# Optimization experiments

Measured on AMD Instinct MI355X. Metric: run time of the kernel, lower is better.

Reference implementation:

```python
import jax, jax.numpy as jnp
import numpy as np

N_NODES = 50000
N_EDGES = 600000
DIM = 128
VOCAB = 512
PAD_ID = 0
LN_EPS = 1e-5


def setup_inputs() -> dict:
    key = jax.random.key(0)
    ks = jax.random.split(key, 8)
    node_ids = jax.random.randint(ks[0], (N_NODES,), 0, VOCAB, dtype=jnp.int32)
    edge_index = jax.random.randint(ks[1], (2, N_EDGES), 0, N_NODES, dtype=jnp.int32)
    edge_weight = jax.random.uniform(ks[2], (N_EDGES,), dtype=jnp.float32)
    # embedding with padding row zeroed (padding_idx semantics)
    emb = jax.random.normal(ks[3], (VOCAB, DIM), dtype=jnp.float32) * 0.05
    emb = emb.at[PAD_ID].set(0.0)
    s = 1.0 / np.sqrt(DIM)
    W1 = jax.random.normal(ks[4], (DIM, DIM), dtype=jnp.float32) * s
    b1 = jnp.zeros((DIM,), jnp.float32)
    W2 = jax.random.normal(ks[5], (DIM, DIM), dtype=jnp.float32) * s
    b2 = jnp.zeros((DIM,), jnp.float32)
    return {
        "node_ids": node_ids, "edge_index": edge_index, "edge_weight": edge_weight,
        "emb": emb, "W1": W1, "b1": b1, "W2": W2, "b2": b2,
        "gamma1": jnp.ones((DIM,), jnp.float32), "beta1": jnp.zeros((DIM,), jnp.float32),
        "gamma2": jnp.ones((DIM,), jnp.float32), "beta2": jnp.zeros((DIM,), jnp.float32),
    }


def _gcn_conv(x, row, col, ew, W, b, n_nodes):
    """PyG GCNConv: normalize=True, add_self_loops=True, improved=False.
    Aggregation j->i: edge (row=src j, col=dst i)."""
    h = x @ W  # [N, out]
    # add self loops with weight 1
    loop = jnp.arange(n_nodes, dtype=row.dtype)
    row_f = jnp.concatenate([row, loop])
    col_f = jnp.concatenate([col, loop])
    ew_f = jnp.concatenate([ew, jnp.ones((n_nodes,), ew.dtype)])
    # symmetric degree normalization (deg over destination index)
    deg = jax.ops.segment_sum(ew_f, col_f, num_segments=n_nodes)
    dis = jnp.where(deg > 0, jax.lax.rsqrt(jnp.maximum(deg, 1e-12)), 0.0)
    norm = dis[row_f] * ew_f * dis[col_f]  # [E+N]
    msg = norm[:, None] * h[row_f]  # gather + scale  [E+N, out]
    out = jax.ops.segment_sum(msg, col_f, num_segments=n_nodes)  # scatter-add
    return out + b


def _layer_norm(x, gamma, beta):
    mu = jnp.mean(x, axis=-1, keepdims=True)
    var = jnp.mean(jnp.square(x - mu), axis=-1, keepdims=True)
    return (x - mu) * jax.lax.rsqrt(var + LN_EPS) * gamma + beta


def reference(node_ids, edge_index, edge_weight, emb, W1, b1, W2, b2,
              gamma1, beta1, gamma2, beta2):
    row, col = edge_index[0], edge_index[1]
    x = emb[node_ids]  # [N, D]
    x1 = _gcn_conv(x, row, col, edge_weight, W1, b1, N_NODES)
    x = _layer_norm(x + x1, gamma1, beta1)  # dropout is identity in eval
    x2 = _gcn_conv(x, row, col, edge_weight, W2, b2, N_NODES)
    x = _layer_norm(x + x2, gamma2, beta2)
    return x
```

## Files before the change

kernel.cpp:

```cpp
#include <hip/hip_runtime.h>

#define N_NODES 50000
#define N_EDGES 600000
#define DIM     128
#define VOCAB   512
#define LN_EPS  1e-5f
#define FIXS    16777216.0f

typedef unsigned int uint;
typedef unsigned long long ull;
typedef unsigned short ushort;
typedef __attribute__((ext_vector_type(8))) short s8v;
typedef __attribute__((ext_vector_type(4))) float f4v;

__device__ __forceinline__ uint f2bf(float f) {
    uint u = __float_as_uint(f);
    return (u + 0x7fffu + ((u >> 16) & 1u)) >> 16;
}
__device__ __forceinline__ float bf_lo(uint p) { return __uint_as_float(p << 16); }
__device__ __forceinline__ float bf_hi(uint p) { return __uint_as_float(p & 0xffff0000u); }

__global__ void deg_rank_kernel(const int* __restrict__ ei, const float* __restrict__ ew,
                                ull* pack, int* __restrict__ rank, int E) {
    int e0 = (blockIdx.x * blockDim.x + threadIdx.x) * 4;
    if (e0 >= E) return;
    int4   c = *(const int4*)  (ei + E + e0);
    float4 w = *(const float4*)(ew + e0);
    ull a0 = (1ull << 32) | (ull)(uint)__float2int_rn(w.x * FIXS);
    ull a1 = (1ull << 32) | (ull)(uint)__float2int_rn(w.y * FIXS);
    ull a2 = (1ull << 32) | (ull)(uint)__float2int_rn(w.z * FIXS);
    ull a3 = (1ull << 32) | (ull)(uint)__float2int_rn(w.w * FIXS);
    ull r0 = atomicAdd(&pack[c.x], a0);
    ull r1 = atomicAdd(&pack[c.y], a1);
    ull r2 = atomicAdd(&pack[c.z], a2);
    ull r3 = atomicAdd(&pack[c.w], a3);
    *(int4*)(rank + e0) = make_int4((int)(r0 >> 32), (int)(r1 >> 32),
                                    (int)(r2 >> 32), (int)(r3 >> 32));
}

__global__ void scan_a(const ull* __restrict__ pack,
                       float* dis, int* row_ptr, int* bsum, int n) {
    __shared__ int sd[1024];
    int t = threadIdx.x;
    int i = blockIdx.x * 1024 + t;
    int v = 0;
    if (i < n) {
        ull pv = pack[i];
        v = (int)(pv >> 32);
        dis[i] = rsqrtf(1.0f + (float)(uint)(pv & 0xffffffffu) * (1.0f / FIXS));
    }
    sd[t] = v;
    __syncthreads();
    for (int off = 1; off < 1024; off <<= 1) {
        int add = (t >= off) ? sd[t - off] : 0;
        __syncthreads();
        sd[t] += add;
        __syncthreads();
    }
    if (i < n) row_ptr[i] = sd[t] - v;
    if (t == 1023) bsum[blockIdx.x] = sd[t];
}

__global__ void scan_b(const int* __restrict__ bsum, int* bofs, int nb) {
    int t = threadIdx.x;
    int v = (t < nb) ? bsum[t] : 0;
    int incl = v;
    #pragma unroll
    for (int off = 1; off < 64; off <<= 1) {
        int up = __shfl_up(incl, off, 64);
        if (t >= off) incl += up;
    }
    if (t < nb) bofs[t] = incl - v;
}

__global__ void scan_c(int* row_ptr, const int* __restrict__ bofs, int n, int E) {
    int i = blockIdx.x * 1024 + threadIdx.x;
    if (i < n) row_ptr[i] += bofs[blockIdx.x];
    if (i == 0) row_ptr[n] = E;
}

__global__ void scatter_kernel(const int* __restrict__ ei, const float* __restrict__ ew,
                               const float* __restrict__ dis, const int* __restrict__ nid,
                               const int* __restrict__ row_ptr, const int* __restrict__ rank,
                               int2* __restrict__ epack, int E) {
    int e = blockIdx.x * blockDim.x + threadIdx.x;
    if (e < E) {
        int s = ei[e];
        int c = ei[E + e];
        int pos = row_ptr[c] + rank[e];
        uint ids = (uint)s | ((uint)nid[s] << 16);
        float wp = dis[s] * ew[e];
        epack[pos] = make_int2((int)ids, __float_as_int(wp));
    }
}

__global__ void prepack_w(const float* __restrict__ W, ushort* __restrict__ Wp) {
    int o = blockIdx.x * 256 + threadIdx.x;
    int j = o & 7, lane = (o >> 3) & 63, chunk = o >> 9;
    int kc = chunk & 3, nc = chunk >> 2;
    int k = kc * 32 + (lane >> 4) * 8 + j;
    int n = nc * 16 + (lane & 15);
    Wp[o] = (ushort)f2bf(W[k * 128 + n]);
}

__global__ __launch_bounds__(256) void matmul128(const float* __restrict__ X,
                                                 const float* __restrict__ W,
                                                 uint* __restrict__ Hb, int M) {
    __shared__ float Wt[32 * 128];
    __shared__ float Xt[64 * 36];
    int tid = threadIdx.x;
    int tx = tid & 31, ty = tid >> 5;
    int r0 = blockIdx.x * 64;
    float acc[8][4];
    #pragma unroll
    for (int j = 0; j < 8; j++)
        #pragma unroll
        for (int c = 0; c < 4; c++) acc[j][c] = 0.f;

    for (int kb = 0; kb < 128; kb += 32) {
        __syncthreads();
        #pragma unroll
        for (int q = 0; q < 4; q++) {
            int f = q * 256 + tid;
            ((float4*)Wt)[f] = *(const float4*)(W + kb * 128 + f * 4);
        }
        #pragma unroll
        for (int q = 0; q < 2; q++) {
            int f = q * 256 + tid;
            int row = f >> 3, cs = f & 7;
            int gr = r0 + row;
            float4 xv = make_float4(0.f, 0.f, 0.f, 0.f);
            if (gr < M) xv = *(const float4*)(X + (size_t)gr * 128 + kb + cs * 4);
            *(float4*)(Xt + row * 36 + cs * 4) = xv;
        }
        __syncthreads();
        #pragma unroll
        for (int k = 0; k < 32; k += 4) {
            float wv[4][4];
            #pragma unroll
            for (int kk = 0; kk < 4; kk++) {
                float4 t4 = *(const float4*)(Wt + (k + kk) * 128 + tx * 4);
                wv[kk][0] = t4.x; wv[kk][1] = t4.y; wv[kk][2] = t4.z; wv[kk][3] = t4.w;
            }
            #pragma unroll
            for (int j = 0; j < 8; j++) {
                float4 xv = *(const float4*)(Xt + (ty * 8 + j) * 36 + k);
                float xs[4] = {xv.x, xv.y, xv.z, xv.w};
                #pragma unroll
                for (int kk = 0; kk < 4; kk++)
                    #pragma unroll
                    for (int c = 0; c < 4; c++)
                        acc[j][c] = fmaf(xs[kk], wv[kk][c], acc[j][c]);
            }
        }
    }
    #pragma unroll
    for (int j = 0; j < 8; j++) {
        int gr = r0 + ty * 8 + j;
        if (gr < M) {
            uint p0 = f2bf(acc[j][0]) | (f2bf(acc[j][1]) << 16);
            uint p1 = f2bf(acc[j][2]) | (f2bf(acc[j][3]) << 16);
            ((uint2*)Hb)[(size_t)gr * 32 + tx] = make_uint2(p0, p1);
        }
    }
}

__global__ __launch_bounds__(256) void mm2_mfma(const uint* __restrict__ Xb,
                                                const ushort* __restrict__ Wp,
                                                ushort* __restrict__ H, int M) {
    int wid = (blockIdx.x * 256 + threadIdx.x) >> 6;
    int lane = threadIdx.x & 63;
    int r0 = wid * 16;
    if (r0 >= M) return;
    int quad = lane >> 4, lo = lane & 15;
    const uint* xrow = Xb + (size_t)(r0 + lo) * 64 + quad * 4;
    s8v a[4];
    #pragma unroll
    for (int kc = 0; kc < 4; kc++) a[kc] = *(const s8v*)(xrow + kc * 16);
    #pragma unroll
    for (int nc = 0; nc < 8; nc++) {
        f4v acc = {0.f, 0.f, 0.f, 0.f};
        #pragma unroll
        for (int kc = 0; kc < 4; kc++) {
            s8v b = *(const s8v*)(Wp + (size_t)((nc * 4 + kc) * 64 + lane) * 8);
            acc = __builtin_amdgcn_mfma_f32_16x16x32_bf16(a[kc], b, acc, 0, 0, 0);
        }
        ushort* hp = H + (size_t)(r0 + quad * 4) * 128 + nc * 16 + lo;
        #pragma unroll
        for (int r = 0; r < 4; r++)
            hp[(size_t)r * 128] = (ushort)f2bf(acc[r]);
    }
}

template<int SHIFT, bool RESID_BF, bool OUT_BF>
__global__ __launch_bounds__(256) void agg_ln(const int* __restrict__ row_ptr,
                                              const int2* __restrict__ epack,
                                              const float* __restrict__ dis,
                                              const uint* __restrict__ hb,
                                              const int* __restrict__ nid,
                                              const void* __restrict__ resid,
                                              const float* __restrict__ bias,
                                              const float* __restrict__ gamma,
                                              const float* __restrict__ beta,
                                              void* __restrict__ out, int n) {
    int i = (blockIdx.x * 256 + threadIdx.x) >> 6;
    int lane = threadIdx.x & 63;
    if (i >= n) return;
    int hri = nid ? nid[i] : i;
    float dl = dis[i];
    uint ps = hb[(size_t)hri * 64 + lane];
    float sx[4] = {dl * bf_lo(ps), 0.f, 0.f, 0.f};
    float sy[4] = {dl * bf_hi(ps), 0.f, 0.f, 0.f};
    int e0 = row_ptr[i], e1 = row_ptr[i + 1];
    for (int j = e0; j < e1; j += 8) {
        int2 er[8];
        #pragma unroll
        for (int k = 0; k < 8; k++) {
            int idx = (j + k < e1) ? j + k : e0;
            er[k] = epack[idx];
        }
        uint qv[8];
        #pragma unroll
        for (int k = 0; k < 8; k++)
            qv[k] = hb[(size_t)(((uint)er[k].x >> SHIFT) & 0xffffu) * 64 + lane];
        #pragma unroll
        for (int k = 0; k < 8; k++) {
            float w = (j + k < e1) ? __int_as_float(er[k].y) : 0.f;
            sx[k & 3] += w * bf_lo(qv[k]);
            sy[k & 3] += w * bf_hi(qv[k]);
        }
    }
    float acc0 = (sx[0] + sx[1]) + (sx[2] + sx[3]);
    float acc1 = (sy[0] + sy[1]) + (sy[2] + sy[3]);
    float2 xr;
    if (RESID_BF) {
        uint pr = ((const uint*)resid)[(size_t)hri * 64 + lane];
        xr = make_float2(bf_lo(pr), bf_hi(pr));
    } else {
        xr = ((const float2*)resid)[(size_t)hri * 64 + lane];
    }
    float2 bi = ((const float2*)bias)[lane];
    float v0 = xr.x + dl * acc0 + bi.x;
    float v1 = xr.y + dl * acc1 + bi.y;
    float s1 = v0 + v1, s2 = v0 * v0 + v1 * v1;
    #pragma unroll
    for (int o = 32; o > 0; o >>= 1) {
        s1 += __shfl_xor(s1, o, 64);
        s2 += __shfl_xor(s2, o, 64);
    }
    float mu   = s1 * (1.0f / DIM);
    float var  = s2 * (1.0f / DIM) - mu * mu;
    float rstd = rsqrtf(var + LN_EPS);
    float2 ga = ((const float2*)gamma)[lane];
    float2 be = ((const float2*)beta)[lane];
    float o0 = (v0 - mu) * rstd * ga.x + be.x;
    float o1 = (v1 - mu) * rstd * ga.y + be.y;
    if (OUT_BF) {
        ((uint*)out)[(size_t)i * 64 + lane] = f2bf(o0) | (f2bf(o1) << 16);
    } else {
        ((float2*)out)[(size_t)i * 64 + lane] = make_float2(o0, o1);
    }
}

extern "C" void kernel_launch(void* const* d_in, const int* in_sizes, int n_in,
                              void* d_out, int out_size, void* d_ws, size_t ws_size,
                              hipStream_t stream) {
    const int*   node_ids = (const int*)  d_in[0];
    const int*   ei       = (const int*)  d_in[1];
    const float* ew       = (const float*)d_in[2];
    const float* emb      = (const float*)d_in[3];
    const float* W1       = (const float*)d_in[4];
    const float* b1       = (const float*)d_in[5];
    const float* W2       = (const float*)d_in[6];
    const float* b2       = (const float*)d_in[7];
    const float* g1       = (const float*)d_in[8];
    const float* be1      = (const float*)d_in[9];
    const float* g2       = (const float*)d_in[10];
    const float* be2      = (const float*)d_in[11];
    float* out = (float*)d_out;

    char* p = (char*)d_ws;
    auto alloc = [&](size_t bytes) {
        char* r = p;
        p += (bytes + 255) & ~(size_t)255;
        return r;
    };
    uint*   h2b     = (uint*)  alloc((size_t)N_NODES * 64 * 4);
    uint*   x1b     = (uint*)  alloc((size_t)N_NODES * 64 * 4);
    uint*   hembB   = (uint*)  alloc((size_t)VOCAB * 64 * 4);
    ushort* Wp      = (ushort*)alloc((size_t)128 * 128 * 2);
    ull*    pack    = (ull*)   alloc((size_t)N_NODES * 8);
    float*  disv    = (float*) alloc((size_t)N_NODES * 4);
    int*    row_ptr = (int*)   alloc((size_t)(N_NODES + 1) * 4);
    int*    rank    = (int*)   alloc((size_t)N_EDGES * 4);
    int*    bsum    = (int*)   alloc(64 * 4);
    int*    bofs    = (int*)   alloc(64 * 4);
    int2*   epack   = (int2*)  alloc((size_t)N_EDGES * 8);

    int nb = (N_NODES + 1023) / 1024;

    hipMemsetAsync(pack, 0, (size_t)N_NODES * 8, stream);
    deg_rank_kernel<<<(N_EDGES / 4 + 255) / 256, 256, 0, stream>>>(ei, ew, pack, rank, N_EDGES);
    scan_a<<<nb, 1024, 0, stream>>>(pack, disv, row_ptr, bsum, N_NODES);
    scan_b<<<1, 64, 0, stream>>>(bsum, bofs, nb);
    scan_c<<<nb, 1024, 0, stream>>>(row_ptr, bofs, N_NODES, N_EDGES);
    scatter_kernel<<<(N_EDGES + 255) / 256, 256, 0, stream>>>(ei, ew, disv, node_ids,
                                                              row_ptr, rank, epack, N_EDGES);
    prepack_w<<<64, 256, 0, stream>>>(W2, Wp);

    matmul128<<<(VOCAB + 63) / 64, 256, 0, stream>>>(emb, W1, hembB, VOCAB);
    agg_ln<16, false, true><<<(N_NODES + 3) / 4, 256, 0, stream>>>(
        row_ptr, epack, disv, hembB, node_ids, emb, b1, g1, be1, x1b, N_NODES);

    mm2_mfma<<<(N_NODES / 16 + 3) / 4, 256, 0, stream>>>(x1b, Wp, (ushort*)h2b, N_NODES);
    agg_ln<0, true, false><<<(N_NODES + 3) / 4, 256, 0, stream>>>(
        row_ptr, epack, disv, h2b, nullptr, x1b, b2, g2, be2, out, N_NODES);
}
```

Before: 242.2 us.

## Merge small kernels, shrink rank to 16-bit, add nontemporal loads/stores

Folds scan_b into scan_c, with each block reducing the preceding block sums itself, and merges the W2 prepack into the first matmul launch, which removes two kernel launches. The per-edge rank array becomes 16-bit and deg_rank now handles 8 edges per thread, halving rank traffic. This assumes no node has 65536 or more in-edges. It also uses readfirstlane for per-node scalars in agg_ln and nontemporal hints on streaming loads and stores, which may hurt cache reuse on epack and residual reads.

```diff
diff --git a/kernel.cpp b/kernel.cpp
--- a/kernel.cpp
+++ b/kernel.cpp
@@ -12,6 +12,11 @@
 typedef unsigned short ushort;
 typedef __attribute__((ext_vector_type(8))) short s8v;
 typedef __attribute__((ext_vector_type(4))) float f4v;
+typedef __attribute__((ext_vector_type(4))) int   i4v;
+typedef __attribute__((ext_vector_type(4))) uint  u4v;
+typedef __attribute__((ext_vector_type(2))) int   i2v;
+typedef __attribute__((ext_vector_type(4))) float fv4;
+typedef __attribute__((ext_vector_type(2))) float f2v;
 
 __device__ __forceinline__ uint f2bf(float f) {
     uint u = __float_as_uint(f);
@@ -21,21 +26,27 @@
 __device__ __forceinline__ float bf_hi(uint p) { return __uint_as_float(p & 0xffff0000u); }
 
 __global__ void deg_rank_kernel(const int* __restrict__ ei, const float* __restrict__ ew,
-                                ull* pack, int* __restrict__ rank, int E) {
-    int e0 = (blockIdx.x * blockDim.x + threadIdx.x) * 4;
+                                ull* pack, ushort* __restrict__ rank, int E) {
+    int e0 = (blockIdx.x * blockDim.x + threadIdx.x) * 8;
     if (e0 >= E) return;
-    int4   c = *(const int4*)  (ei + E + e0);
-    float4 w = *(const float4*)(ew + e0);
-    ull a0 = (1ull << 32) | (ull)(uint)__float2int_rn(w.x * FIXS);
-    ull a1 = (1ull << 32) | (ull)(uint)__float2int_rn(w.y * FIXS);
-    ull a2 = (1ull << 32) | (ull)(uint)__float2int_rn(w.z * FIXS);
-    ull a3 = (1ull << 32) | (ull)(uint)__float2int_rn(w.w * FIXS);
-    ull r0 = atomicAdd(&pack[c.x], a0);
-    ull r1 = atomicAdd(&pack[c.y], a1);
-    ull r2 = atomicAdd(&pack[c.z], a2);
-    ull r3 = atomicAdd(&pack[c.w], a3);
-    *(int4*)(rank + e0) = make_int4((int)(r0 >> 32), (int)(r1 >> 32),
-                                    (int)(r2 >> 32), (int)(r3 >> 32));
+    i4v c0 = __builtin_nontemporal_load((const i4v*)(ei + E + e0));
+    i4v c1 = __builtin_nontemporal_load((const i4v*)(ei + E + e0 + 4));
+    fv4 w0 = __builtin_nontemporal_load((const fv4*)(ew + e0));
+    fv4 w1 = __builtin_nontemporal_load((const fv4*)(ew + e0 + 4));
+    int   c[8] = {c0.x, c0.y, c0.z, c0.w, c1.x, c1.y, c1.z, c1.w};
+    float w[8] = {w0.x, w0.y, w0.z, w0.w, w1.x, w1.y, w1.z, w1.w};
+    ull r[8];
+    #pragma unroll
+    for (int k = 0; k < 8; k++) {
+        ull a = (1ull << 32) | (ull)(uint)__float2int_rn(w[k] * FIXS);
+        r[k] = atomicAdd(&pack[c[k]], a);
+    }
+    u4v o;
+    o.x = (uint)(r[0] >> 32) | ((uint)(r[1] >> 32) << 16);
+    o.y = (uint)(r[2] >> 32) | ((uint)(r[3] >> 32) << 16);
+    o.z = (uint)(r[4] >> 32) | ((uint)(r[5] >> 32) << 16);
+    o.w = (uint)(r[6] >> 32) | ((uint)(r[7] >> 32) << 16);
+    __builtin_nontemporal_store(o, (u4v*)(rank + e0));
 }
 
 __global__ void scan_a(const ull* __restrict__ pack,
@@ -61,54 +72,56 @@
     if (t == 1023) bsum[blockIdx.x] = sd[t];
 }
 
-__global__ void scan_b(const int* __restrict__ bsum, int* bofs, int nb) {
+__global__ void scan_c(int* row_ptr, const int* __restrict__ bsum,
+                       int n, int E, int nb) {
+    __shared__ int ofs_s;
     int t = threadIdx.x;
-    int v = (t < nb) ? bsum[t] : 0;
-    int incl = v;
-    #pragma unroll
-    for (int off = 1; off < 64; off <<= 1) {
-        int up = __shfl_up(incl, off, 64);
-        if (t >= off) incl += up;
-    }
-    if (t < nb) bofs[t] = incl - v;
-}
-
-__global__ void scan_c(int* row_ptr, const int* __restrict__ bofs, int n, int E) {
-    int i = blockIdx.x * 1024 + threadIdx.x;
-    if (i < n) row_ptr[i] += bofs[blockIdx.x];
+    if (t < 64) {
+        int v = (t < nb && t < (int)blockIdx.x) ? bsum[t] : 0;
+        #pragma unroll
+        for (int o = 32; o > 0; o >>= 1) v += __shfl_xor(v, o, 64);
+        if (t == 0) ofs_s = v;
+    }
+    __syncthreads();
+    int i = blockIdx.x * 1024 + t;
+    if (i < n) row_ptr[i] += ofs_s;
     if (i == 0) row_ptr[n] = E;
 }
 
 __global__ void scatter_kernel(const int* __restrict__ ei, const float* __restrict__ ew,
                                const float* __restrict__ dis, const int* __restrict__ nid,
-                               const int* __restrict__ row_ptr, const int* __restrict__ rank,
+                               const int* __restrict__ row_ptr, const ushort* __restrict__ rank,
                                int2* __restrict__ epack, int E) {
     int e = blockIdx.x * blockDim.x + threadIdx.x;
     if (e < E) {
         int s = ei[e];
         int c = ei[E + e];
-        int pos = row_ptr[c] + rank[e];
+        int pos = row_ptr[c] + (int)rank[e];
         uint ids = (uint)s | ((uint)nid[s] << 16);
         float wp = dis[s] * ew[e];
-        epack[pos] = make_int2((int)ids, __float_as_int(wp));
-    }
-}
-
-__global__ void prepack_w(const float* __restrict__ W, ushort* __restrict__ Wp) {
-    int o = blockIdx.x * 256 + threadIdx.x;
-    int j = o & 7, lane = (o >> 3) & 63, chunk = o >> 9;
-    int kc = chunk & 3, nc = chunk >> 2;
-    int k = kc * 32 + (lane >> 4) * 8 + j;
-    int n = nc * 16 + (lane & 15);
-    Wp[o] = (ushort)f2bf(W[k * 128 + n]);
-}
-
-__global__ __launch_bounds__(256) void matmul128(const float* __restrict__ X,
-                                                 const float* __restrict__ W,
-                                                 uint* __restrict__ Hb, int M) {
+        i2v rec = {(int)ids, __float_as_int(wp)};
+        __builtin_nontemporal_store(rec, (i2v*)(epack + pos));
+    }
+}
+
+__global__ __launch_bounds__(256) void mm1_prepack(const float* __restrict__ X,
+                                                   const float* __restrict__ W,
+                                                   uint* __restrict__ Hb, int M,
+                                                   const float* __restrict__ W2,
+                                                   ushort* __restrict__ Wp) {
     __shared__ float Wt[32 * 128];
     __shared__ float Xt[64 * 36];
     int tid = threadIdx.x;
+    int nmm = (M + 63) / 64;
+    if ((int)blockIdx.x >= nmm) {
+        int o = (blockIdx.x - nmm) * 256 + tid;
+        int j = o & 7, lane = (o >> 3) & 63, chunk = o >> 9;
+        int kc = chunk & 3, nc = chunk >> 2;
+        int k = kc * 32 + (lane >> 4) * 8 + j;
+        int n = nc * 16 + (lane & 15);
+        Wp[o] = (ushort)f2bf(W2[k * 128 + n]);
+        return;
+    }
     int tx = tid & 31, ty = tid >> 5;
     int r0 = blockIdx.x * 64;
     float acc[8][4];
@@ -206,18 +219,19 @@
     int i = (blockIdx.x * 256 + threadIdx.x) >> 6;
     int lane = threadIdx.x & 63;
     if (i >= n) return;
-    int hri = nid ? nid[i] : i;
-    float dl = dis[i];
+    int iw = __builtin_amdgcn_readfirstlane(i);
+    int hri = nid ? nid[iw] : iw;
+    float dl = dis[iw];
     uint ps = hb[(size_t)hri * 64 + lane];
     float sx[4] = {dl * bf_lo(ps), 0.f, 0.f, 0.f};
     float sy[4] = {dl * bf_hi(ps), 0.f, 0.f, 0.f};
-    int e0 = row_ptr[i], e1 = row_ptr[i + 1];
+    int e0 = row_ptr[iw], e1 = row_ptr[iw + 1];
     for (int j = e0; j < e1; j += 8) {
-        int2 er[8];
+        i2v er[8];
         #pragma unroll
         for (int k = 0; k < 8; k++) {
             int idx = (j + k < e1) ? j + k : e0;
-            er[k] = epack[idx];
+            er[k] = __builtin_nontemporal_load((const i2v*)(epack + idx));
         }
         uint qv[8];
         #pragma unroll
@@ -234,7 +248,7 @@
     float acc1 = (sy[0] + sy[1]) + (sy[2] + sy[3]);
     float2 xr;
     if (RESID_BF) {
-        uint pr = ((const uint*)resid)[(size_t)hri * 64 + lane];
+        uint pr = __builtin_nontemporal_load((const uint*)resid + (size_t)hri * 64 + lane);
         xr = make_float2(bf_lo(pr), bf_hi(pr));
     } else {
         xr = ((const float2*)resid)[(size_t)hri * 64 + lane];
@@ -256,9 +270,11 @@
     float o0 = (v0 - mu) * rstd * ga.x + be.x;
     float o1 = (v1 - mu) * rstd * ga.y + be.y;
     if (OUT_BF) {
-        ((uint*)out)[(size_t)i * 64 + lane] = f2bf(o0) | (f2bf(o1) << 16);
+        __builtin_nontemporal_store(f2bf(o0) | (f2bf(o1) << 16),
+                                    (uint*)out + (size_t)i * 64 + lane);
     } else {
-        ((float2*)out)[(size_t)i * 64 + lane] = make_float2(o0, o1);
+        f2v ov = {o0, o1};
+        __builtin_nontemporal_store(ov, (f2v*)((float2*)out + (size_t)i * 64 + lane));
     }
 }
 
@@ -292,23 +308,20 @@
     ull*    pack    = (ull*)   alloc((size_t)N_NODES * 8);
     float*  disv    = (float*) alloc((size_t)N_NODES * 4);
     int*    row_ptr = (int*)   alloc((size_t)(N_NODES + 1) * 4);
-    int*    rank    = (int*)   alloc((size_t)N_EDGES * 4);
+    ushort* rank    = (ushort*)alloc((size_t)N_EDGES * 2);
     int*    bsum    = (int*)   alloc(64 * 4);
-    int*    bofs    = (int*)   alloc(64 * 4);
     int2*   epack   = (int2*)  alloc((size_t)N_EDGES * 8);
 
     int nb = (N_NODES + 1023) / 1024;
 
-    hipMemsetAsync(pack, 0, (size_t)N_NODES * 8, stream);
-    deg_rank_kernel<<<(N_EDGES / 4 + 255) / 256, 256, 0, stream>>>(ei, ew, pack, rank, N_EDGES);
+    (void)hipMemsetAsync(pack, 0, (size_t)N_NODES * 8, stream);
+    deg_rank_kernel<<<(N_EDGES / 8 + 255) / 256, 256, 0, stream>>>(ei, ew, pack, rank, N_EDGES);
     scan_a<<<nb, 1024, 0, stream>>>(pack, disv, row_ptr, bsum, N_NODES);
-    scan_b<<<1, 64, 0, stream>>>(bsum, bofs, nb);
-    scan_c<<<nb, 1024, 0, stream>>>(row_ptr, bofs, N_NODES, N_EDGES);
+    scan_c<<<nb, 1024, 0, stream>>>(row_ptr, bsum, N_NODES, N_EDGES, nb);
     scatter_kernel<<<(N_EDGES + 255) / 256, 256, 0, stream>>>(ei, ew, disv, node_ids,
                                                               row_ptr, rank, epack, N_EDGES);
-    prepack_w<<<64, 256, 0, stream>>>(W2, Wp);
-
-    matmul128<<<(VOCAB + 63) / 64, 256, 0, stream>>>(emb, W1, hembB, VOCAB);
+
+    mm1_prepack<<<(VOCAB + 63) / 64 + 64, 256, 0, stream>>>(emb, W1, hembB, VOCAB, W2, Wp);
     agg_ln<16, false, true><<<(N_NODES + 3) / 4, 256, 0, stream>>>(
         row_ptr, epack, disv, hembB, node_ids, emb, b1, g1, be1, x1b, N_NODES);
 
```

Result: faster. 226.4 us (-6.5%).
